# Performance work log

Measured on AMD Instinct MI355X. Metric: run time of the kernel, lower is better.

## Reference

```python
import jax, jax.numpy as jnp
import numpy as np
from jax import lax

T_STEPS = 1024
BATCH = 1024
NUM_STATES = 64


def setup_inputs() -> dict:
    key = jax.random.key(0)
    k_em, k_len, k_start, k_stop, k_trans = jax.random.split(key, 5)
    emission_factors = jax.random.normal(k_em, (T_STEPS, BATCH, NUM_STATES), dtype=jnp.float32)
    sequence_sizes = jax.random.randint(k_len, (BATCH,), 1, T_STEPS + 1, dtype=jnp.int32)
    start_factors = jax.random.normal(k_start, (NUM_STATES,), dtype=jnp.float32)
    stop_factors = jax.random.normal(k_stop, (NUM_STATES,), dtype=jnp.float32)
    transition_factors = jax.random.normal(k_trans, (NUM_STATES, NUM_STATES), dtype=jnp.float32)
    return {
        "emission_factors": emission_factors,
        "sequence_sizes": sequence_sizes,
        "start_factors": start_factors,
        "stop_factors": stop_factors,
        "transition_factors": transition_factors,
    }


def reference(emission_factors, sequence_sizes, start_factors, stop_factors, transition_factors):
    # emission_factors: [T, B, S] time-major; sequence_sizes: [B] lengths in [1, T].
    # Linear-chain CRF forward algorithm (log-partition):
    #   alpha_0   = start + em_0
    #   alpha_t[s] = logsumexp_p(alpha_{t-1}[p] + trans[s, p]) + em_t[s]   (while active)
    #   log_Z     = logsumexp_s(alpha_{L-1}[s] + stop[s])
    # Masked scan: alpha is frozen once a sequence ends, matching the packed
    # variable-batch-size iteration of the original (penultimate_alphas).
    max_steps = emission_factors.shape[0]

    alpha0 = start_factors[None, :] + emission_factors[0]  # [B, S]
    # active[t-1, b] = (t < length_b) for t = 1..T-1
    active = (jnp.arange(1, max_steps)[:, None] < sequence_sizes[None, :])[:, :, None]  # [T-1, B, 1]

    def step(alpha, inp):
        em_t, act = inp  # em_t: [B, S], act: [B, 1]
        # alpha[b, None, p] + trans[None, s, p] -> logsumexp over p
        new_alpha = jax.nn.logsumexp(alpha[:, None, :] + transition_factors[None, :, :], axis=2) + em_t
        return jnp.where(act, new_alpha, alpha), None

    alpha, _ = lax.scan(step, alpha0, (emission_factors[1:], active))
    log_normalizer = jax.nn.logsumexp(alpha + stop_factors[None, :], axis=1)  # [B]
    return log_normalizer
```

## Files before the change

### kernel.cpp

```cpp
#include <hip/hip_runtime.h>

#define T_STEPS 1024
#define BATCH   1024
#define NS      64

__global__ __launch_bounds__(64)
__attribute__((amdgpu_waves_per_eu(1, 1)))
void crf_fwd_v6(const float* __restrict__ em,
                const int*   __restrict__ seqlen,
                const float* __restrict__ start,
                const float* __restrict__ stop,
                const float* __restrict__ trans,
                float*       __restrict__ out) {
    __shared__ float us4[NS] __attribute__((aligned(16)));
    const int b = blockIdx.x;
    const int s = threadIdx.x;
    const int L = seqlen[b];
    const int total = L - 1;

    float e[NS];
    {
        const float4* t4 = reinterpret_cast<const float4*>(trans + s * NS);
        #pragma unroll
        for (int i = 0; i < NS / 4; ++i) {
            float4 t = t4[i];
            e[4 * i + 0] = __expf(t.x);
            e[4 * i + 1] = __expf(t.y);
            e[4 * i + 2] = __expf(t.z);
            e[4 * i + 3] = __expf(t.w);
        }
    }
    #pragma unroll
    for (int i = 0; i < NS; ++i) asm volatile("" : "+v"(e[i]));

    float u = __expf(start[s] + em[(size_t)b * NS + s]);
    float c = 0.f;
    const float*  gp = em + (size_t)b * NS + s;
    const size_t  TS = (size_t)BATCH * NS;

    auto step = [&](float ex, bool rn) {
        if (rn) {
            float m = __uint_as_float(__builtin_amdgcn_readlane(__float_as_uint(u), 0));
            m = fmaxf(m, 1e-30f);
            ex *= __builtin_amdgcn_rcpf(m);
            c += __logf(m);
        }
        us4[s] = u;
        float a0 = 0.f, a1 = 0.f, a2 = 0.f, a3 = 0.f;
        #pragma unroll
        for (int i = 0; i < NS / 4; ++i) {
            float4 q = *reinterpret_cast<const float4*>(&us4[4 * i]);
            a0 = fmaf(e[4 * i + 0], q.x, a0);
            a1 = fmaf(e[4 * i + 1], q.y, a1);
            a2 = fmaf(e[4 * i + 2], q.z, a2);
            a3 = fmaf(e[4 * i + 3], q.w, a3);
        }
        u = ((a0 + a1) + (a2 + a3)) * ex;
    };

    float emq[8];
    #pragma unroll
    for (int j = 0; j < 8; ++j) {
        int t = 1 + j; if (t > T_STEPS - 1) t = T_STEPS - 1;
        emq[j] = gp[(size_t)t * TS];
    }

    int done = 0;
    while (done + 8 <= total) {
        float emn[8];
        #pragma unroll
        for (int j = 0; j < 8; ++j) {
            int t = done + 9 + j; if (t > T_STEPS - 1) t = T_STEPS - 1;
            emn[j] = gp[(size_t)t * TS];
        }
        float ex[8];
        #pragma unroll
        for (int j = 0; j < 8; ++j) ex[j] = __expf(emq[j]);

        step(ex[0], true);  step(ex[1], false); step(ex[2], false); step(ex[3], false);
        step(ex[4], true);  step(ex[5], false); step(ex[6], false); step(ex[7], false);

        #pragma unroll
        for (int j = 0; j < 8; ++j) emq[j] = emn[j];
        done += 8;
    }

    const int tail = total - done;
    for (int j = 0; j < tail; ++j)
        step(__expf(emq[j]), (j & 3) == 0);

    float v = u * __expf(stop[s]);
    #pragma unroll
    for (int o = 1; o < 64; o <<= 1) v += __shfl_xor(v, o, 64);
    if (s == 0) out[b] = __logf(v) + c;
}

extern "C" void kernel_launch(void* const* d_in, const int* in_sizes, int n_in,
                              void* d_out, int out_size, void* d_ws, size_t ws_size,
                              hipStream_t stream) {
    const float* em     = (const float*)d_in[0];
    const int*   seqlen = (const int*)  d_in[1];
    const float* start  = (const float*)d_in[2];
    const float* stop   = (const float*)d_in[3];
    const float* trans  = (const float*)d_in[4];
    float*       out    = (float*)d_out;

    crf_fwd_v6<<<BATCH, NS, 0, stream>>>(em, seqlen, start, stop, trans, out);
}
```

Measured before the change: 615.6 us.

## Replace LDS broadcast of alpha with DPP row-rotate and swizzle lane exchanges

The per-step matrix-vector product no longer stores alpha to shared memory and reads it back as float4 broadcasts. Each lane instead obtains the other lanes' values through ds_swizzle, shfl_xor across halves, and DPP row_ror operand modifiers fused into the FMAs. The transition-exp register layout is permuted at setup to match the rotation pattern, which is probed at runtime via DPP. This aims to remove LDS store/load latency and barriers from the serial recurrence, at the cost of cross-lane permute ops (shfl is still an LDS-path bpermute) and more VALU instructions.

```diff
diff --git a/kernel.cpp b/kernel.cpp
--- a/kernel.cpp
+++ b/kernel.cpp
@@ -4,15 +4,33 @@
 #define BATCH   1024
 #define NS      64
 
+#define ROW_ROR(R) (0x120 | (R))
+#define SWZ_XOR16 0x401F
+
+#define FMA_DPP(uq, EB, R)                                                    \
+    { int t_ = __builtin_amdgcn_update_dpp((int)(uq), (int)(uq),              \
+                                           ROW_ROR(R), 0xF, 0xF, true);       \
+      a[(R) & 3] = fmaf(__uint_as_float((unsigned)t_), e[(EB) + (R)],         \
+                        a[(R) & 3]); }
+
+#define FMA_Q(uq, EB)                                                         \
+    a[0] = fmaf(__uint_as_float((unsigned)(uq)), e[(EB)], a[0]);              \
+    FMA_DPP(uq, EB, 1)  FMA_DPP(uq, EB, 2)  FMA_DPP(uq, EB, 3)                \
+    FMA_DPP(uq, EB, 4)  FMA_DPP(uq, EB, 5)  FMA_DPP(uq, EB, 6)                \
+    FMA_DPP(uq, EB, 7)  FMA_DPP(uq, EB, 8)  FMA_DPP(uq, EB, 9)                \
+    FMA_DPP(uq, EB, 10) FMA_DPP(uq, EB, 11) FMA_DPP(uq, EB, 12)               \
+    FMA_DPP(uq, EB, 13) FMA_DPP(uq, EB, 14) FMA_DPP(uq, EB, 15)
+
+#define PROBE(R) d[R] = __builtin_amdgcn_update_dpp(s, s, ROW_ROR(R), 0xF, 0xF, true);
+
 __global__ __launch_bounds__(64)
 __attribute__((amdgpu_waves_per_eu(1, 1)))
-void crf_fwd_v6(const float* __restrict__ em,
+void crf_fwd_v7(const float* __restrict__ em,
                 const int*   __restrict__ seqlen,
                 const float* __restrict__ start,
                 const float* __restrict__ stop,
                 const float* __restrict__ trans,
                 float*       __restrict__ out) {
-    __shared__ float us4[NS] __attribute__((aligned(16)));
     const int b = blockIdx.x;
     const int s = threadIdx.x;
     const int L = seqlen[b];
@@ -20,15 +38,17 @@
 
     float e[NS];
     {
-        const float4* t4 = reinterpret_cast<const float4*>(trans + s * NS);
+        int d[16];
+        d[0] = s;
+        PROBE(1)  PROBE(2)  PROBE(3)  PROBE(4)  PROBE(5)
+        PROBE(6)  PROBE(7)  PROBE(8)  PROBE(9)  PROBE(10)
+        PROBE(11) PROBE(12) PROBE(13) PROBE(14) PROBE(15)
+        const float* tr = trans + s * NS;
         #pragma unroll
-        for (int i = 0; i < NS / 4; ++i) {
-            float4 t = t4[i];
-            e[4 * i + 0] = __expf(t.x);
-            e[4 * i + 1] = __expf(t.y);
-            e[4 * i + 2] = __expf(t.z);
-            e[4 * i + 3] = __expf(t.w);
-        }
+        for (int q = 0; q < 4; ++q)
+            #pragma unroll
+            for (int r = 0; r < 16; ++r)
+                e[q * 16 + r] = __expf(tr[d[r] ^ (q << 4)]);
     }
     #pragma unroll
     for (int i = 0; i < NS; ++i) asm volatile("" : "+v"(e[i]));
@@ -45,17 +65,16 @@
             ex *= __builtin_amdgcn_rcpf(m);
             c += __logf(m);
         }
-        us4[s] = u;
-        float a0 = 0.f, a1 = 0.f, a2 = 0.f, a3 = 0.f;
-        #pragma unroll
-        for (int i = 0; i < NS / 4; ++i) {
-            float4 q = *reinterpret_cast<const float4*>(&us4[4 * i]);
-            a0 = fmaf(e[4 * i + 0], q.x, a0);
-            a1 = fmaf(e[4 * i + 1], q.y, a1);
-            a2 = fmaf(e[4 * i + 2], q.z, a2);
-            a3 = fmaf(e[4 * i + 3], q.w, a3);
-        }
-        u = ((a0 + a1) + (a2 + a3)) * ex;
+        const int u0 = (int)__float_as_uint(u);
+        const int u1 = __builtin_amdgcn_ds_swizzle(u0, SWZ_XOR16);
+        const int u2 = __shfl_xor(u0, 32, 64);
+        const int u3 = __shfl_xor(u1, 32, 64);
+        float a[4] = {0.f, 0.f, 0.f, 0.f};
+        FMA_Q(u0,  0)
+        FMA_Q(u1, 16)
+        FMA_Q(u2, 32)
+        FMA_Q(u3, 48)
+        u = ((a[0] + a[1]) + (a[2] + a[3])) * ex;
     };
 
     float emq[8];
@@ -105,5 +124,5 @@
     const float* trans  = (const float*)d_in[4];
     float*       out    = (float*)d_out;
 
-    crf_fwd_v6<<<BATCH, NS, 0, stream>>>(em, seqlen, start, stop, trans, out);
+    crf_fwd_v7<<<BATCH, NS, 0, stream>>>(em, seqlen, start, stop, trans, out);
 }
```

Measured after the change: 535.6 us. -13.0%, faster.

## Batch 16 chains per wave and compute CRF recurrence with bf16 MFMA

Applied to the files above, without the earlier changes.

Replaces the one-sequence-per-block scalar FMA recurrence with a wave that handles 16 sequences at once. Each step is a 64x64 by 64x16 product done with bf16 MFMA instructions, and the state vector is exchanged through swizzled LDS. Every chain runs the full 1024 steps and records its result when its own length is reached, which removes per-block length variance but does redundant work for short sequences. The bf16 transition and state values cut precision, and there are 64 blocks instead of 1024, which risks poor GPU occupancy.

```diff
diff --git a/kernel.cpp b/kernel.cpp
--- a/kernel.cpp
+++ b/kernel.cpp
@@ -3,96 +3,181 @@
 #define T_STEPS 1024
 #define BATCH   1024
 #define NS      64
+#define CPB     16
+#define NBLK    (BATCH / CPB)
+#define TS      ((size_t)BATCH * NS)
+
+typedef __attribute__((ext_vector_type(8))) __bf16 bf16x8;
+typedef __attribute__((ext_vector_type(4))) __bf16 bf16x4;
+typedef __attribute__((ext_vector_type(4))) float  f32x4;
+
+#define SWZ_XOR16 0x401F
+__device__ __forceinline__ float swz16f(float x) {
+    return __uint_as_float((unsigned)__builtin_amdgcn_ds_swizzle(
+        (int)__float_as_uint(x), SWZ_XOR16));
+}
 
 __global__ __launch_bounds__(64)
-__attribute__((amdgpu_waves_per_eu(1, 1)))
-void crf_fwd_v6(const float* __restrict__ em,
+void crf_fwd_v9(const float* __restrict__ em,
                 const int*   __restrict__ seqlen,
                 const float* __restrict__ start,
                 const float* __restrict__ stop,
                 const float* __restrict__ trans,
                 float*       __restrict__ out) {
-    __shared__ float us4[NS] __attribute__((aligned(16)));
-    const int b = blockIdx.x;
-    const int s = threadIdx.x;
-    const int L = seqlen[b];
-    const int total = L - 1;
+    __shared__ __align__(16) char Ulds[CPB * 128];
 
-    float e[NS];
-    {
-        const float4* t4 = reinterpret_cast<const float4*>(trans + s * NS);
-        #pragma unroll
-        for (int i = 0; i < NS / 4; ++i) {
-            float4 t = t4[i];
-            e[4 * i + 0] = __expf(t.x);
-            e[4 * i + 1] = __expf(t.y);
-            e[4 * i + 2] = __expf(t.z);
-            e[4 * i + 3] = __expf(t.w);
+    const int l  = threadIdx.x;
+    const int c  = l & 15;
+    const int g  = l >> 4;
+    const int b0 = blockIdx.x * CPB;
+    const int Lc = seqlen[b0 + c];
+    const int c7 = c & 7;
+
+    bf16x8 ae[4][2];
+#pragma unroll
+    for (int mt = 0; mt < 4; ++mt)
+#pragma unroll
+        for (int ks = 0; ks < 2; ++ks) {
+            const float* tp = trans + (size_t)(16 * mt + c) * NS + 32 * ks + 8 * g;
+            f32x4 t0 = *(const f32x4*)tp;
+            f32x4 t1 = *(const f32x4*)(tp + 4);
+            bf16x8 a;
+            a[0] = (__bf16)__expf(t0[0]); a[1] = (__bf16)__expf(t0[1]);
+            a[2] = (__bf16)__expf(t0[2]); a[3] = (__bf16)__expf(t0[3]);
+            a[4] = (__bf16)__expf(t1[0]); a[5] = (__bf16)__expf(t1[1]);
+            a[6] = (__bf16)__expf(t1[2]); a[7] = (__bf16)__expf(t1[3]);
+            ae[mt][ks] = a;
         }
-    }
-    #pragma unroll
-    for (int i = 0; i < NS; ++i) asm volatile("" : "+v"(e[i]));
 
-    float u = __expf(start[s] + em[(size_t)b * NS + s]);
-    float c = 0.f;
-    const float*  gp = em + (size_t)b * NS + s;
-    const size_t  TS = (size_t)BATCH * NS;
-
-    auto step = [&](float ex, bool rn) {
-        if (rn) {
-            float m = __uint_as_float(__builtin_amdgcn_readlane(__float_as_uint(u), 0));
-            m = fmaxf(m, 1e-30f);
-            ex *= __builtin_amdgcn_rcpf(m);
-            c += __logf(m);
-        }
-        us4[s] = u;
-        float a0 = 0.f, a1 = 0.f, a2 = 0.f, a3 = 0.f;
-        #pragma unroll
-        for (int i = 0; i < NS / 4; ++i) {
-            float4 q = *reinterpret_cast<const float4*>(&us4[4 * i]);
-            a0 = fmaf(e[4 * i + 0], q.x, a0);
-            a1 = fmaf(e[4 * i + 1], q.y, a1);
-            a2 = fmaf(e[4 * i + 2], q.z, a2);
-            a3 = fmaf(e[4 * i + 3], q.w, a3);
-        }
-        u = ((a0 + a1) + (a2 + a3)) * ex;
-    };
-
-    float emq[8];
-    #pragma unroll
-    for (int j = 0; j < 8; ++j) {
-        int t = 1 + j; if (t > T_STEPS - 1) t = T_STEPS - 1;
-        emq[j] = gp[(size_t)t * TS];
+    float es[4][4], st0[4][4];
+#pragma unroll
+    for (int mt = 0; mt < 4; ++mt) {
+        f32x4 sv = *(const f32x4*)(stop  + 16 * mt + 4 * g);
+        f32x4 tv = *(const f32x4*)(start + 16 * mt + 4 * g);
+#pragma unroll
+        for (int i = 0; i < 4; ++i) { es[mt][i] = __expf(sv[i]); st0[mt][i] = tv[i]; }
     }
 
-    int done = 0;
-    while (done + 8 <= total) {
-        float emn[8];
-        #pragma unroll
-        for (int j = 0; j < 8; ++j) {
-            int t = done + 9 + j; if (t > T_STEPS - 1) t = T_STEPS - 1;
-            emn[j] = gp[(size_t)t * TS];
-        }
-        float ex[8];
-        #pragma unroll
-        for (int j = 0; j < 8; ++j) ex[j] = __expf(emq[j]);
+    char* ub = (char*)Ulds;
+    int woff[4], boff[2];
+#pragma unroll
+    for (int mt = 0; mt < 4; ++mt)
+        woff[mt] = c * 128 + ((((2 * mt + (g >> 1)) ^ c7) << 4) | ((g & 1) << 3));
+#pragma unroll
+    for (int ks = 0; ks < 2; ++ks)
+        boff[ks] = c * 128 + (((4 * ks + g) ^ c7) << 4);
 
-        step(ex[0], true);  step(ex[1], false); step(ex[2], false); step(ex[3], false);
-        step(ex[4], true);  step(ex[5], false); step(ex[6], false); step(ex[7], false);
+    const float* emp[4];
+#pragma unroll
+    for (int mt = 0; mt < 4; ++mt)
+        emp[mt] = em + (size_t)(b0 + c) * NS + 16 * mt + 4 * g;
 
-        #pragma unroll
-        for (int j = 0; j < 8; ++j) emq[j] = emn[j];
-        done += 8;
+    f32x4 emb[4][4];
+#pragma unroll
+    for (int S = 0; S < 4; ++S)
+#pragma unroll
+        for (int mt = 0; mt < 4; ++mt)
+            emb[S][mt] = *(const f32x4*)(emp[mt] + (size_t)S * TS);
+
+#define CAPTURE_BODY(T_)                                                      \
+    do {                                                                      \
+        float dv = 0.f;                                                       \
+        _Pragma("unroll") for (int m_ = 0; m_ < 4; ++m_)                      \
+            _Pragma("unroll") for (int i_ = 0; i_ < 4; ++i_)                  \
+                dv = fmaf(u[m_][i_], es[m_][i_], dv);                         \
+        dv += swz16f(dv);                                                     \
+        dv += __shfl_xor(dv, 32, 64);                                         \
+        if ((T_) == Lc - 1 && g == 0) out[b0 + c] = __logf(dv) + c_acc;       \
+    } while (0)
+
+#define WRITE_READ()                                                          \
+    do {                                                                      \
+        bf16x4 p0, p1;                                                        \
+        p0[0] = (__bf16)u[0][0]; p0[1] = (__bf16)u[0][1];                     \
+        p0[2] = (__bf16)u[0][2]; p0[3] = (__bf16)u[0][3];                     \
+        p1[0] = (__bf16)u[1][0]; p1[1] = (__bf16)u[1][1];                     \
+        p1[2] = (__bf16)u[1][2]; p1[3] = (__bf16)u[1][3];                     \
+        *(bf16x4*)(ub + woff[0]) = p0;                                        \
+        *(bf16x4*)(ub + woff[1]) = p1;                                        \
+        bfA = *(bf16x8*)(ub + boff[0]);                                       \
+        p0[0] = (__bf16)u[2][0]; p0[1] = (__bf16)u[2][1];                     \
+        p0[2] = (__bf16)u[2][2]; p0[3] = (__bf16)u[2][3];                     \
+        p1[0] = (__bf16)u[3][0]; p1[1] = (__bf16)u[3][1];                     \
+        p1[2] = (__bf16)u[3][2]; p1[3] = (__bf16)u[3][3];                     \
+        *(bf16x4*)(ub + woff[2]) = p0;                                        \
+        *(bf16x4*)(ub + woff[3]) = p1;                                        \
+        bfB = *(bf16x8*)(ub + boff[1]);                                       \
+    } while (0)
+
+#define STEP(T_, SLOT_, RN_, LAST_)                                           \
+    do {                                                                      \
+        f32x4 zz = {0.f, 0.f, 0.f, 0.f};                                      \
+        f32x4 acc[4];                                                         \
+        _Pragma("unroll") for (int m_ = 0; m_ < 4; ++m_)                      \
+            acc[m_] = __builtin_amdgcn_mfma_f32_16x16x32_bf16(                \
+                ae[m_][0], bfA, zz, 0, 0, 0);                                 \
+        _Pragma("unroll") for (int m_ = 0; m_ < 4; ++m_)                      \
+            acc[m_] = __builtin_amdgcn_mfma_f32_16x16x32_bf16(                \
+                ae[m_][1], bfB, acc[m_], 0, 0, 0);                            \
+        if (RN_) {                                                            \
+            float v1 = fmaxf(mloc, swz16f(mloc));                             \
+            float mm = fmaxf(v1, __shfl_xor(v1, 32, 64));                     \
+            mm  = fmaxf(mm, 1e-30f);                                          \
+            inv = __builtin_amdgcn_rcpf(mm);                                  \
+            c_acc += __logf(mm);                                              \
+        }                                                                     \
+        _Pragma("unroll") for (int m_ = 0; m_ < 4; ++m_)                      \
+            _Pragma("unroll") for (int i_ = 0; i_ < 4; ++i_) {                \
+                float exv = __expf(emb[SLOT_][m_][i_]);                       \
+                if (RN_) exv *= inv;                                          \
+                u[m_][i_] = acc[m_][i_] * exv;                                \
+            }                                                                 \
+        {        \
+            size_t tn = (size_t)(((T_) + 4 <= T_STEPS - 1) ? (T_) + 4         \
+                                                           : T_STEPS - 1);    \
+            _Pragma("unroll") for (int m_ = 0; m_ < 4; ++m_)                  \
+                emb[SLOT_][m_] = *(const f32x4*)(emp[m_] + tn * TS);          \
+        }                                                                     \
+        if (__any((T_) == Lc - 1)) CAPTURE_BODY(T_);                          \
+        if (LAST_) {                                                          \
+            mloc = u[0][0];                                                   \
+            _Pragma("unroll") for (int m_ = 0; m_ < 4; ++m_)                  \
+                _Pragma("unroll") for (int i_ = 0; i_ < 4; ++i_)              \
+                    mloc = fmaxf(mloc, u[m_][i_]);                            \
+        }                                                                     \
+        WRITE_READ();                                                         \
+    } while (0)
+
+    float u[4][4];
+#pragma unroll
+    for (int mt = 0; mt < 4; ++mt)
+#pragma unroll
+        for (int i = 0; i < 4; ++i)
+            u[mt][i] = __expf(st0[mt][i] + emb[0][mt][i]);
+#pragma unroll
+    for (int mt = 0; mt < 4; ++mt)
+        emb[0][mt] = *(const f32x4*)(emp[mt] + 4 * TS);
+
+    float c_acc = 0.f, inv = 1.f;
+    (void)inv;
+    if (__any(0 == Lc - 1)) CAPTURE_BODY(0);
+
+    float mloc = u[0][0];
+#pragma unroll
+    for (int mt = 0; mt < 4; ++mt)
+#pragma unroll
+        for (int i = 0; i < 4; ++i) mloc = fmaxf(mloc, u[mt][i]);
+
+    bf16x8 bfA, bfB;
+    WRITE_READ();
+
+    for (int grp = 0; grp < 256; ++grp) {
+        const int t0_ = 1 + 4 * grp;
+        STEP(t0_ + 0, 1, 1, 0);
+        STEP(t0_ + 1, 2, 0, 0);
+        STEP(t0_ + 2, 3, 0, 0);
+        STEP(t0_ + 3, 0, 0, 1);
     }
-
-    const int tail = total - done;
-    for (int j = 0; j < tail; ++j)
-        step(__expf(emq[j]), (j & 3) == 0);
-
-    float v = u * __expf(stop[s]);
-    #pragma unroll
-    for (int o = 1; o < 64; o <<= 1) v += __shfl_xor(v, o, 64);
-    if (s == 0) out[b] = __logf(v) + c;
 }
 
 extern "C" void kernel_launch(void* const* d_in, const int* in_sizes, int n_in,
@@ -105,5 +190,5 @@
     const float* trans  = (const float*)d_in[4];
     float*       out    = (float*)d_out;
 
-    crf_fwd_v6<<<BATCH, NS, 0, stream>>>(em, seqlen, start, stop, trans, out);
+    crf_fwd_v9<<<NBLK, 64, 0, stream>>>(em, seqlen, start, stop, trans, out);
 }
```

Measured after the change: 568.0 us. 1.08x faster.
